# Kernel tuning notes

Measured on AMD Instinct MI355X. Metric: run time of the kernel, lower is better.

## Reference

```python
import jax, jax.numpy as jnp
import numpy as np

NUM_HEADS = 8


def setup_inputs() -> dict:
    key0 = jax.random.key(0)
    ks = jax.random.split(key0, 12)
    N, M, B, C = 512, 512, 1, 256
    inp = {
        "query": jax.random.normal(ks[0], (N, B, C), dtype=jnp.float32),
        "key": jax.random.normal(ks[1], (M, B, C), dtype=jnp.float32),
        "value": jax.random.normal(ks[2], (M, B, C), dtype=jnp.float32),
        "embed_g": jax.random.normal(ks[3], (B, N, M, C), dtype=jnp.float32),
        "Wq": jax.random.normal(ks[4], (C, C), dtype=jnp.float32) * 0.02,
        "bq": jnp.zeros((C,), dtype=jnp.float32),
        "Wk": jax.random.normal(ks[5], (C, C), dtype=jnp.float32) * 0.02,
        "bk": jnp.zeros((C,), dtype=jnp.float32),
        "Wv": jax.random.normal(ks[6], (C, C), dtype=jnp.float32) * 0.02,
        "bv": jnp.zeros((C,), dtype=jnp.float32),
        "Wg": jax.random.normal(ks[7], (C, C), dtype=jnp.float32) * 0.02,
        "bg": jnp.zeros((C,), dtype=jnp.float32),
    }
    return inp


def reference(query, key, value, embed_g, Wq, bq, Wk, bk, Wv, bv, Wg, bg):
    H = NUM_HEADS
    N, B, C = query.shape
    M = key.shape[0]
    Dh = C // H

    # torch nn.Linear: x @ W.T + b
    q = (query @ Wq.T + bq).reshape(N, B, H, Dh).transpose(1, 2, 0, 3)   # (B,H,N,Dh)
    k = (key @ Wk.T + bk).reshape(M, B, H, Dh).transpose(1, 2, 0, 3)     # (B,H,M,Dh)
    v = (value @ Wv.T + bv).reshape(M, B, H, Dh).transpose(1, 2, 0, 3)   # (B,H,M,Dh)
    g = (embed_g @ Wg.T + bg).reshape(B, N, M, H, Dh).transpose(0, 3, 1, 2, 4)  # (B,H,N,M,Dh)

    scores_p = jnp.einsum('bhnc,bhnmc->bhnm', q, g)
    scores_e = jnp.einsum('bhnc,bhmc->bhnm', q, k)
    scores = (scores_e + scores_p) / jnp.sqrt(jnp.asarray(Dh, dtype=q.dtype))
    attn = jax.nn.softmax(scores, axis=-1)                               # (B,H,N,M)

    hidden = jnp.einsum('bhnm,bhmd->bhnd', attn, v)                      # (B,H,N,Dh)
    hidden = hidden.transpose(0, 2, 1, 3).reshape(B, N, C)               # (B,N,C)
    hidden = hidden.transpose(1, 0, 2)                                   # (N,B,C)
    return hidden, attn
```

## Files before the change

kernel.cpp:

```cpp
#include <hip/hip_runtime.h>


template <int CTRL, int RMASK>
__device__ __forceinline__ float dpp_add(float v) {
  int x = __builtin_amdgcn_update_dpp(0, __float_as_int(v), CTRL, RMASK, 0xf, false);
  return v + __int_as_float(x);
}

__global__ __launch_bounds__(256) void k_transpose(const float* __restrict__ Wq,
                                                   const float* __restrict__ Wk,
                                                   const float* __restrict__ Wv,
                                                   float* __restrict__ wt) {
  const float* W = (blockIdx.y == 0) ? Wq : (blockIdx.y == 1) ? Wk : Wv;
  float* O = wt + (size_t)blockIdx.y * 65536;
  __shared__ float t[64][65];
  const int tile = blockIdx.x;
  const int tr = (tile >> 2) * 64, tc = (tile & 3) * 64;
  const int c = threadIdx.x & 63, r0 = threadIdx.x >> 6;
#pragma unroll
  for (int i = 0; i < 16; ++i) {
    int r = r0 + i * 4;
    t[r][c] = W[(tr + r) * 256 + tc + c];
  }
  __syncthreads();
#pragma unroll
  for (int i = 0; i < 16; ++i) {
    int r = r0 + i * 4;
    O[(tc + r) * 256 + tr + c] = t[c][r];
  }
}

__global__ __launch_bounds__(256) void k_proj(const float* __restrict__ q_in,
                                              const float* __restrict__ k_in,
                                              const float* __restrict__ v_in,
                                              const float* __restrict__ bq,
                                              const float* __restrict__ bk,
                                              const float* __restrict__ bv,
                                              const float* __restrict__ wt,
                                              float* __restrict__ outb) {
  const int mat = blockIdx.y;
  const float* x = mat == 0 ? q_in : mat == 1 ? k_in : v_in;
  const float* b = mat == 0 ? bq : mat == 1 ? bk : bv;
  const float* WT = wt + (size_t)mat * 65536;
  float* out = outb + (size_t)mat * 131072;

  __shared__ float xl[8][256];
  const int tid = threadIdx.x;
  const int n0 = blockIdx.x * 8;
  for (int idx = tid; idx < 2048; idx += 256)
    xl[idx >> 8][idx & 255] = x[(n0 + (idx >> 8)) * 256 + (idx & 255)];
  __syncthreads();

  float acc[8] = {0.f, 0.f, 0.f, 0.f, 0.f, 0.f, 0.f, 0.f};
  for (int j = 0; j < 256; j += 4) {
    const float w0 = WT[(j + 0) * 256 + tid];
    const float w1 = WT[(j + 1) * 256 + tid];
    const float w2 = WT[(j + 2) * 256 + tid];
    const float w3 = WT[(j + 3) * 256 + tid];
#pragma unroll
    for (int r = 0; r < 8; ++r) {
      const float4 xv = *(const float4*)&xl[r][j];
      acc[r] += xv.x * w0 + xv.y * w1 + xv.z * w2 + xv.w * w3;
    }
  }
  const float bb = b[tid];
#pragma unroll
  for (int r = 0; r < 8; ++r) out[(n0 + r) * 256 + tid] = acc[r] + bb;
}

__global__ __launch_bounds__(256) void k_tfold(const float* __restrict__ qkv,
                                               const float* __restrict__ Wg,
                                               float* __restrict__ t_ws) {
  const int h = blockIdx.y;
  const int n0 = blockIdx.x * 64;
  const int tid = threadIdx.x;
  const float scale = 0.17677669529663687f;
  __shared__ float wg_s[32][256];
  __shared__ float qs[64][32];

  for (int idx = tid; idx < 8192; idx += 256)
    wg_s[idx >> 8][idx & 255] = Wg[(size_t)(h * 32 + (idx >> 8)) * 256 + (idx & 255)];
  for (int idx = tid; idx < 2048; idx += 256)
    qs[idx >> 5][idx & 31] = qkv[(size_t)(n0 + (idx >> 5)) * 256 + h * 32 + (idx & 31)];
  __syncthreads();

  float wr[32];
#pragma unroll
  for (int i = 0; i < 32; ++i) wr[i] = wg_s[i][tid];
  for (int nn = 0; nn < 64; ++nn) {
    float a = 0.f;
#pragma unroll
    for (int i = 0; i < 32; ++i) a = fmaf(qs[nn][i], wr[i], a);
    t_ws[(size_t)(n0 + nn) * 2048 + h * 256 + tid] = a * scale;
  }
}

__global__ __launch_bounds__(512, 4) void k_main(const float* __restrict__ Eg,
                                                 const float* __restrict__ qkv,
                                                 const float* __restrict__ t_ws,
                                                 float* __restrict__ out) {
  const float* k_g = qkv + 131072;
  const float* v_g = qkv + 262144;
  const int n = blockIdx.x;
  const int tid = threadIdx.x;
  const int lane = tid & 63, w = tid >> 6;
  const int s = lane & 31, g = lane >> 5;
  const int hd = s >> 2;
  const float scale = 0.17677669529663687f;
  float* attn = out + 131072;

  __shared__ float sc[8 * 520];
  __shared__ float invd[8];
  __shared__ float pv2[8 * 260];

  float t_r[8][8];
#pragma unroll
  for (int h = 0; h < 8; ++h) {
    const float4 a = *(const float4*)(t_ws + (size_t)n * 2048 + h * 256 + s * 8);
    const float4 b = *(const float4*)(t_ws + (size_t)n * 2048 + h * 256 + s * 8 + 4);
    t_r[h][0] = a.x; t_r[h][1] = a.y; t_r[h][2] = a.z; t_r[h][3] = a.w;
    t_r[h][4] = b.x; t_r[h][5] = b.y; t_r[h][6] = b.z; t_r[h][7] = b.w;
  }
  float q_r[8];
  {
    const float4 a = *(const float4*)(qkv + n * 256 + s * 8);
    const float4 b = *(const float4*)(qkv + n * 256 + s * 8 + 4);
    q_r[0] = a.x * scale; q_r[1] = a.y * scale; q_r[2] = a.z * scale; q_r[3] = a.w * scale;
    q_r[4] = b.x * scale; q_r[5] = b.y * scale; q_r[6] = b.z * scale; q_r[7] = b.w * scale;
  }

  const float* E0 = Eg + ((size_t)n * 512 + w * 64 + g) * 256 + s * 8;
  const float* K0 = k_g + (size_t)(w * 64 + g) * 256 + s * 8;

#pragma unroll 4
  for (int it = 0; it < 32; ++it) {
    const float4 e0 = *(const float4*)(E0);
    const float4 e1 = *(const float4*)(E0 + 4);
    const float4 k0 = *(const float4*)(K0);
    const float4 k1 = *(const float4*)(K0 + 4);
    float kacc;
    kacc = k0.x * q_r[0];             kacc = fmaf(k0.y, q_r[1], kacc);
    kacc = fmaf(k0.z, q_r[2], kacc);  kacc = fmaf(k0.w, q_r[3], kacc);
    kacc = fmaf(k1.x, q_r[4], kacc);  kacc = fmaf(k1.y, q_r[5], kacc);
    kacc = fmaf(k1.z, q_r[6], kacc);  kacc = fmaf(k1.w, q_r[7], kacc);
    const int m = w * 64 + it * 2 + g;
    float vout = 0.f;
#pragma unroll
    for (int h = 0; h < 8; ++h) {
      float v = (hd == h) ? kacc : 0.f;
      v = fmaf(e0.x, t_r[h][0], v); v = fmaf(e0.y, t_r[h][1], v);
      v = fmaf(e0.z, t_r[h][2], v); v = fmaf(e0.w, t_r[h][3], v);
      v = fmaf(e1.x, t_r[h][4], v); v = fmaf(e1.y, t_r[h][5], v);
      v = fmaf(e1.z, t_r[h][6], v); v = fmaf(e1.w, t_r[h][7], v);
      v = dpp_add<0xB1, 0xf>(v);
      v = dpp_add<0x4E, 0xf>(v);
      v = dpp_add<0x141, 0xf>(v);
      v = dpp_add<0x140, 0xf>(v);
      v = dpp_add<0x142, 0xa>(v);
      vout = (s == 16 + h) ? v : vout;
    }
    if ((unsigned)(s - 16) < 8u) sc[(s - 16) * 520 + m] = vout;
    E0 += 512; K0 += 512;
  }
  __syncthreads();

  {
    float vals[8];
#pragma unroll
    for (int i = 0; i < 8; ++i) vals[i] = sc[w * 520 + lane + i * 64];
    float mx = vals[0];
#pragma unroll
    for (int i = 1; i < 8; ++i) mx = fmaxf(mx, vals[i]);
#pragma unroll
    for (int off = 1; off < 64; off <<= 1) mx = fmaxf(mx, __shfl_xor(mx, off));
    float sum = 0.f;
#pragma unroll
    for (int i = 0; i < 8; ++i) {
      const float e = __expf(vals[i] - mx);
      sum += e;
      sc[w * 520 + lane + i * 64] = e;
    }
#pragma unroll
    for (int off = 1; off < 64; off <<= 1) sum += __shfl_xor(sum, off);
    if (lane == 0) invd[w] = 1.f / sum;
  }
  __syncthreads();

#pragma unroll
  for (int r = 0; r < 8; ++r) {
    const int idx = tid + r * 512;
    const int h = idx >> 9, mm = idx & 511;
    attn[(size_t)h * 262144 + n * 512 + mm] = sc[h * 520 + mm] * invd[h];
  }

  {
    const int c4 = (tid & 63) * 4;
    const int mc = tid >> 6;
    const int hh = (tid & 63) >> 3;
    const float* pr = sc + hh * 520 + mc * 64;
    const float* vp = v_g + (size_t)(mc * 64) * 256 + c4;
    float4 a4 = {0.f, 0.f, 0.f, 0.f};
#pragma unroll 4
    for (int m = 0; m < 64; ++m) {
      const float p = pr[m];
      const float4 v4 = *(const float4*)vp;
      a4.x = fmaf(p, v4.x, a4.x);
      a4.y = fmaf(p, v4.y, a4.y);
      a4.z = fmaf(p, v4.z, a4.z);
      a4.w = fmaf(p, v4.w, a4.w);
      vp += 256;
    }
    *(float4*)&pv2[mc * 260 + c4] = a4;
  }
  __syncthreads();
  if (tid < 256) {
    float acc = 0.f;
#pragma unroll
    for (int mc2 = 0; mc2 < 8; ++mc2) acc += pv2[mc2 * 260 + tid];
    out[n * 256 + tid] = acc * invd[tid >> 5];
  }
}

extern "C" void kernel_launch(void* const* d_in, const int* in_sizes, int n_in,
                              void* d_out, int out_size, void* d_ws, size_t ws_size,
                              hipStream_t stream) {
  const float* query = (const float*)d_in[0];
  const float* key   = (const float*)d_in[1];
  const float* value = (const float*)d_in[2];
  const float* Eg    = (const float*)d_in[3];
  const float* Wq    = (const float*)d_in[4];
  const float* bq    = (const float*)d_in[5];
  const float* Wk    = (const float*)d_in[6];
  const float* bk    = (const float*)d_in[7];
  const float* Wv    = (const float*)d_in[8];
  const float* bv    = (const float*)d_in[9];
  const float* Wg    = (const float*)d_in[10];
  float* out = (float*)d_out;

  float* ws = (float*)d_ws;
  float* wt = ws;
  float* qkv = wt + 3 * 65536;
  float* t_ws = qkv + 3 * 131072;

  k_transpose<<<dim3(16, 3), 256, 0, stream>>>(Wq, Wk, Wv, wt);
  k_proj<<<dim3(64, 3), 256, 0, stream>>>(query, key, value, bq, bk, bv, wt, qkv);
  k_tfold<<<dim3(8, 8), 256, 0, stream>>>(qkv, Wg, t_ws);
  k_main<<<dim3(512), 512, 0, stream>>>(Eg, qkv, t_ws, out);
}
```

Measured before the change: 105.2 us.

## Fuse weight transpose into projection and Wg fold into main kernel

Removes the separate weight-transpose kernel by having the projection kernel stage 32-column tiles of W into padded LDS and read them transposed. Removes the t-fold kernel by computing the per-query q·Wg fold inside the main attention kernel from LDS, so two launches and their global round trips go away. In exchange each main block re-reads the 256 KB Wg (from L2) and does extra prologue arithmetic before streaming embed_g. The projection kernel also gains extra barriers per tile.

```diff
diff --git a/kernel.cpp b/kernel.cpp
--- a/kernel.cpp
+++ b/kernel.cpp
@@ -5,29 +5,6 @@
 __device__ __forceinline__ float dpp_add(float v) {
   int x = __builtin_amdgcn_update_dpp(0, __float_as_int(v), CTRL, RMASK, 0xf, false);
   return v + __int_as_float(x);
-}
-
-__global__ __launch_bounds__(256) void k_transpose(const float* __restrict__ Wq,
-                                                   const float* __restrict__ Wk,
-                                                   const float* __restrict__ Wv,
-                                                   float* __restrict__ wt) {
-  const float* W = (blockIdx.y == 0) ? Wq : (blockIdx.y == 1) ? Wk : Wv;
-  float* O = wt + (size_t)blockIdx.y * 65536;
-  __shared__ float t[64][65];
-  const int tile = blockIdx.x;
-  const int tr = (tile >> 2) * 64, tc = (tile & 3) * 64;
-  const int c = threadIdx.x & 63, r0 = threadIdx.x >> 6;
-#pragma unroll
-  for (int i = 0; i < 16; ++i) {
-    int r = r0 + i * 4;
-    t[r][c] = W[(tr + r) * 256 + tc + c];
-  }
-  __syncthreads();
-#pragma unroll
-  for (int i = 0; i < 16; ++i) {
-    int r = r0 + i * 4;
-    O[(tc + r) * 256 + tr + c] = t[c][r];
-  }
 }
 
 __global__ __launch_bounds__(256) void k_proj(const float* __restrict__ q_in,
@@ -36,68 +13,52 @@
                                               const float* __restrict__ bq,
                                               const float* __restrict__ bk,
                                               const float* __restrict__ bv,
-                                              const float* __restrict__ wt,
+                                              const float* __restrict__ Wq,
+                                              const float* __restrict__ Wk,
+                                              const float* __restrict__ Wv,
                                               float* __restrict__ outb) {
   const int mat = blockIdx.y;
   const float* x = mat == 0 ? q_in : mat == 1 ? k_in : v_in;
   const float* b = mat == 0 ? bq : mat == 1 ? bk : bv;
-  const float* WT = wt + (size_t)mat * 65536;
+  const float* W = mat == 0 ? Wq : mat == 1 ? Wk : Wv;
   float* out = outb + (size_t)mat * 131072;
 
   __shared__ float xl[8][256];
+  __shared__ float wtile[256][33];
   const int tid = threadIdx.x;
   const int n0 = blockIdx.x * 8;
   for (int idx = tid; idx < 2048; idx += 256)
     xl[idx >> 8][idx & 255] = x[(n0 + (idx >> 8)) * 256 + (idx & 255)];
-  __syncthreads();
 
   float acc[8] = {0.f, 0.f, 0.f, 0.f, 0.f, 0.f, 0.f, 0.f};
-  for (int j = 0; j < 256; j += 4) {
-    const float w0 = WT[(j + 0) * 256 + tid];
-    const float w1 = WT[(j + 1) * 256 + tid];
-    const float w2 = WT[(j + 2) * 256 + tid];
-    const float w3 = WT[(j + 3) * 256 + tid];
-#pragma unroll
-    for (int r = 0; r < 8; ++r) {
-      const float4 xv = *(const float4*)&xl[r][j];
-      acc[r] += xv.x * w0 + xv.y * w1 + xv.z * w2 + xv.w * w3;
+  for (int j0 = 0; j0 < 256; j0 += 32) {
+    __syncthreads();
+    for (int idx = tid; idx < 8192; idx += 256) {
+      const int cc = idx >> 5, jj = idx & 31;
+      wtile[cc][jj] = W[cc * 256 + j0 + jj];
+    }
+    __syncthreads();
+#pragma unroll
+    for (int jj = 0; jj < 32; jj += 4) {
+      const float w0 = wtile[tid][jj + 0];
+      const float w1 = wtile[tid][jj + 1];
+      const float w2 = wtile[tid][jj + 2];
+      const float w3 = wtile[tid][jj + 3];
+#pragma unroll
+      for (int r = 0; r < 8; ++r) {
+        const float4 xv = *(const float4*)&xl[r][j0 + jj];
+        acc[r] += xv.x * w0 + xv.y * w1 + xv.z * w2 + xv.w * w3;
+      }
     }
   }
   const float bb = b[tid];
 #pragma unroll
   for (int r = 0; r < 8; ++r) out[(n0 + r) * 256 + tid] = acc[r] + bb;
-}
-
-__global__ __launch_bounds__(256) void k_tfold(const float* __restrict__ qkv,
-                                               const float* __restrict__ Wg,
-                                               float* __restrict__ t_ws) {
-  const int h = blockIdx.y;
-  const int n0 = blockIdx.x * 64;
-  const int tid = threadIdx.x;
-  const float scale = 0.17677669529663687f;
-  __shared__ float wg_s[32][256];
-  __shared__ float qs[64][32];
-
-  for (int idx = tid; idx < 8192; idx += 256)
-    wg_s[idx >> 8][idx & 255] = Wg[(size_t)(h * 32 + (idx >> 8)) * 256 + (idx & 255)];
-  for (int idx = tid; idx < 2048; idx += 256)
-    qs[idx >> 5][idx & 31] = qkv[(size_t)(n0 + (idx >> 5)) * 256 + h * 32 + (idx & 31)];
-  __syncthreads();
-
-  float wr[32];
-#pragma unroll
-  for (int i = 0; i < 32; ++i) wr[i] = wg_s[i][tid];
-  for (int nn = 0; nn < 64; ++nn) {
-    float a = 0.f;
-#pragma unroll
-    for (int i = 0; i < 32; ++i) a = fmaf(qs[nn][i], wr[i], a);
-    t_ws[(size_t)(n0 + nn) * 2048 + h * 256 + tid] = a * scale;
-  }
 }
 
 __global__ __launch_bounds__(512, 4) void k_main(const float* __restrict__ Eg,
                                                  const float* __restrict__ qkv,
-                                                 const float* __restrict__ t_ws,
+                                                 const float* __restrict__ Wg,
                                                  float* __restrict__ out) {
   const float* k_g = qkv + 131072;
   const float* v_g = qkv + 262144;
@@ -109,25 +70,37 @@
   const float scale = 0.17677669529663687f;
   float* attn = out + 131072;
 
+  __shared__ float ql[256];
+  __shared__ float t_lds[2048];
   __shared__ float sc[8 * 520];
   __shared__ float invd[8];
   __shared__ float pv2[8 * 260];
 
+  if (tid < 256) ql[tid] = qkv[n * 256 + tid];
+  __syncthreads();
+  {
+    const int jcol = tid & 255, hb = (tid >> 8) * 4;
+#pragma unroll
+    for (int hh = 0; hh < 4; ++hh) {
+      const int h = hb + hh;
+      float a = 0.f;
+      const float* wg = Wg + (size_t)(h * 32) * 256 + jcol;
+#pragma unroll 8
+      for (int i = 0; i < 32; ++i) a = fmaf(ql[h * 32 + i], wg[(size_t)i * 256], a);
+      t_lds[h * 256 + jcol] = a * scale;
+    }
+  }
+  __syncthreads();
+
   float t_r[8][8];
 #pragma unroll
   for (int h = 0; h < 8; ++h) {
-    const float4 a = *(const float4*)(t_ws + (size_t)n * 2048 + h * 256 + s * 8);
-    const float4 b = *(const float4*)(t_ws + (size_t)n * 2048 + h * 256 + s * 8 + 4);
-    t_r[h][0] = a.x; t_r[h][1] = a.y; t_r[h][2] = a.z; t_r[h][3] = a.w;
-    t_r[h][4] = b.x; t_r[h][5] = b.y; t_r[h][6] = b.z; t_r[h][7] = b.w;
+#pragma unroll
+    for (int c = 0; c < 8; ++c) t_r[h][c] = t_lds[h * 256 + s * 8 + c];
   }
   float q_r[8];
-  {
-    const float4 a = *(const float4*)(qkv + n * 256 + s * 8);
-    const float4 b = *(const float4*)(qkv + n * 256 + s * 8 + 4);
-    q_r[0] = a.x * scale; q_r[1] = a.y * scale; q_r[2] = a.z * scale; q_r[3] = a.w * scale;
-    q_r[4] = b.x * scale; q_r[5] = b.y * scale; q_r[6] = b.z * scale; q_r[7] = b.w * scale;
-  }
+#pragma unroll
+  for (int c = 0; c < 8; ++c) q_r[c] = ql[s * 8 + c] * scale;
 
   const float* E0 = Eg + ((size_t)n * 512 + w * 64 + g) * 256 + s * 8;
   const float* K0 = k_g + (size_t)(w * 64 + g) * 256 + s * 8;
@@ -237,13 +210,8 @@
   const float* Wg    = (const float*)d_in[10];
   float* out = (float*)d_out;
 
-  float* ws = (float*)d_ws;
-  float* wt = ws;
-  float* qkv = wt + 3 * 65536;
-  float* t_ws = qkv + 3 * 131072;
-
-  k_transpose<<<dim3(16, 3), 256, 0, stream>>>(Wq, Wk, Wv, wt);
-  k_proj<<<dim3(64, 3), 256, 0, stream>>>(query, key, value, bq, bk, bv, wt, qkv);
-  k_tfold<<<dim3(8, 8), 256, 0, stream>>>(qkv, Wg, t_ws);
-  k_main<<<dim3(512), 512, 0, stream>>>(Eg, qkv, t_ws, out);
-}
+  float* qkv = (float*)d_ws;
+
+  k_proj<<<dim3(64, 3), 256, 0, stream>>>(query, key, value, bq, bk, bv, Wq, Wk, Wv, qkv);
+  k_main<<<dim3(512), 512, 0, stream>>>(Eg, qkv, Wg, out);
+}
```

Measured after the change: 96.60 us (median of 2 runs). 8.1% less time.
